# Kernel tuning notes

Measured on AMD Instinct MI355X. Metric: run time of the kernel, lower is better.

Reference implementation:

```python
import jax, jax.numpy as jnp
import numpy as np

M1, M2, BS = 2000, 400, 8
AT = M1 + M2
E1, E2, E3 = 60000, 20000, 20000
H, F, NG, L, C = 64, 64, 50, 4, 4
CUTOFF = 10.0
LOG2 = 0.6931471805599453  # shift of ShiftedSoftplus


def _ssp(x):
    return jax.nn.softplus(x) - LOG2


def _smear(d):
    # GaussianSmearing(0, cutoff, NG)
    offset = jnp.linspace(0.0, CUTOFF, NG)
    coeff = -0.5 / (offset[1] - offset[0]) ** 2
    return jnp.exp(coeff * (d[:, None] - offset[None, :]) ** 2)  # [E, NG]


def _colored_mlp(attr, colors, w1, b1, w2, b2):
    # w1:[C,NG,F] b1:[C,F] w2:[C,F,F] b2:[C,F]; route each edge through its color's MLP
    out = jnp.zeros((attr.shape[0], w1.shape[-1]), attr.dtype)
    for c in range(C):  # fixed small color count
        h = _ssp(attr @ w1[c] + b1[c]) @ w2[c] + b2[c]
        out = out + jnp.where((colors == c)[:, None], h, jnp.zeros((), attr.dtype))
    return out


def _block(h, ei, ew, attr, col, p):
    # InteractionBlock: CFConv -> ssp -> linear
    mw1, mb1, mw2, mb2, cw1, cw2, cb2, bw, bb = p
    Ccut = 0.5 * (jnp.cos(ew * jnp.pi / CUTOFF) + 1.0)
    W = _colored_mlp(attr, col, mw1, mb1, mw2, mb2) * Ccut[:, None]  # [E,F]
    x = h @ cw1                                   # lin1 (no bias) [N,F]
    msg = x[ei[:, 0]] * W                         # gather x_j, modulate
    agg = jax.ops.segment_sum(msg, ei[:, 1], num_segments=h.shape[0])  # scatter-add
    x = agg @ cw2 + cb2                           # lin2
    return _ssp(x) @ bw + bb                      # act + block linear


def _batch_graph(ei, ew, col):
    # replicate per-structure edges across the batch with node offset b*AT
    offs = (jnp.arange(BS, dtype=ei.dtype) * AT)[:, None, None]
    ei_b = (ei[None] + offs).reshape(-1, 2)
    return ei_b, jnp.tile(ew, BS), jnp.tile(col, BS)


def _forward(sites, sites_p, e1, ew1, c1, e2, ew2, c2, e3, ew3, c3,
             emb_w, emb_p_w, mlp_w1, mlp_b1, mlp_w2, mlp_b2,
             conv_w1, conv_w2, conv_b2, blk_w, blk_b,
             out_w1, out_b1, out_w2, out_b2):
    h = jnp.concatenate([emb_w[sites], emb_p_w[sites_p]], axis=1).reshape(BS * AT, H)
    graphs = []
    for (ei, ew, col) in ((e1, ew1, c1), (e2, ew2, c2), (e3, ew3, c3)):
        ei_b, ew_b, col_b = _batch_graph(ei, ew, col)
        graphs.append((ei_b, ew_b, col_b, _smear(ew_b)))
    for l in range(L):
        delta = jnp.zeros_like(h)
        for g, (ei_b, ew_b, col_b, attr_b) in enumerate(graphs):
            p = (mlp_w1[l, g], mlp_b1[l, g], mlp_w2[l, g], mlp_b2[l, g],
                 conv_w1[l, g], conv_w2[l, g], conv_b2[l, g], blk_w[l, g], blk_b[l, g])
            delta = delta + _block(h, ei_b, ew_b, attr_b, col_b, p)
        h = h + delta
    hp = h.reshape(BS, AT, H)[:, M1:, :]   # mask selects pore nodes only
    o = hp @ out_w1 + out_b1               # NB: original has `h - self.act(h)` no-op, so no activation here
    o = o @ out_w2 + out_b2                # [BS, M2, 1]
    return o.sum(axis=1)                   # 'add' readout per batch -> [BS, 1]


def setup_inputs() -> dict:
    key = jax.random.key(0)
    ks = jax.random.split(key, 24)
    f = lambda i, shape, s=0.1: jax.random.normal(ks[i], shape, jnp.float32) * s
    sites = jax.random.randint(ks[0], (BS, M1), 0, 1, dtype=jnp.int32)
    sites_p = jax.random.randint(ks[1], (BS, M2), 0, 2, dtype=jnp.int32)
    e1 = jax.random.randint(ks[2], (E1, 2), 0, M1, dtype=jnp.int32)
    e2 = jnp.stack([jax.random.randint(ks[3], (E2,), 0, M1, dtype=jnp.int32),
                    jax.random.randint(ks[4], (E2,), M1, AT, dtype=jnp.int32)], 1)
    e3 = jnp.stack([jax.random.randint(ks[5], (E3,), M1, AT, dtype=jnp.int32),
                    jax.random.randint(ks[6], (E3,), 0, M1, dtype=jnp.int32)], 1)
    ew1 = jax.random.uniform(ks[7], (E1,), jnp.float32, 0.5, CUTOFF)
    ew2 = jax.random.uniform(ks[8], (E2,), jnp.float32, 0.5, CUTOFF)
    ew3 = jax.random.uniform(ks[9], (E3,), jnp.float32, 0.5, CUTOFF)
    c1 = jax.random.randint(ks[10], (E1,), 0, C, dtype=jnp.int32)
    c2 = jax.random.randint(ks[11], (E2,), 0, C, dtype=jnp.int32)
    c3 = jax.random.randint(ks[12], (E3,), 0, C, dtype=jnp.int32)
    return {
        'sites': sites, 'sites_p': sites_p,
        'edge_idx1': e1, 'edge_weight1': ew1, 'colors1': c1,
        'edge_idx2': e2, 'edge_weight2': ew2, 'colors2': c2,
        'edge_idx3': e3, 'edge_weight3': ew3, 'colors3': c3,
        'emb_w': f(13, (1, H), 1.0), 'emb_p_w': f(14, (2, H), 1.0),
        'mlp_w1': f(15, (L, 3, C, NG, F)), 'mlp_b1': jnp.zeros((L, 3, C, F), jnp.float32),
        'mlp_w2': f(16, (L, 3, C, F, F)), 'mlp_b2': jnp.zeros((L, 3, C, F), jnp.float32),
        'conv_w1': f(17, (L, 3, H, F)), 'conv_w2': f(18, (L, 3, F, H)),
        'conv_b2': jnp.zeros((L, 3, H), jnp.float32),
        'blk_w': f(19, (L, 3, H, H)), 'blk_b': jnp.zeros((L, 3, H), jnp.float32),
        'out_w1': f(20, (H, H // 2)), 'out_b1': jnp.zeros((H // 2,), jnp.float32),
        'out_w2': f(21, (H // 2, 1)), 'out_b2': jnp.zeros((1,), jnp.float32),
    }


def reference(sites, sites_p, edge_idx1, edge_weight1, colors1,
              edge_idx2, edge_weight2, colors2, edge_idx3, edge_weight3, colors3,
              emb_w, emb_p_w, mlp_w1, mlp_b1, mlp_w2, mlp_b2,
              conv_w1, conv_w2, conv_b2, blk_w, blk_b,
              out_w1, out_b1, out_w2, out_b2):
    return _forward(sites, sites_p, edge_idx1, edge_weight1, colors1,
                    edge_idx2, edge_weight2, colors2, edge_idx3, edge_weight3, colors3,
                    emb_w, emb_p_w, mlp_w1, mlp_b1, mlp_w2, mlp_b2,
                    conv_w1, conv_w2, conv_b2, blk_w, blk_b,
                    out_w1, out_b1, out_w2, out_b2)
```

## Files before the change

### kernel.cpp

```cpp
#include <hip/hip_runtime.h>
#include <math.h>

constexpr int M1 = 2000, M2 = 400, BS = 8;
constexpr int AT = M1 + M2;
constexpr int NN = BS * AT;
constexpr int E1 = 60000, E2 = 20000, E3 = 20000;
constexpr int ET = E1 + E2 + E3;
constexpr int H = 64, F = 64, NG = 50, L = 4, C = 4;
constexpr float CUTOFF = 10.0f;
constexpr float LOG2F_ = 0.6931471805599453f;

constexpr float SMEAR_STEP = 10.0f / 49.0f;
constexpr float SMEAR_COEFF = -12.005f;
constexpr float PI_OVER_CUT = 0.31415926535897932f;

constexpr int NBLK = (ET + 255) / 256;

constexpr int NT = 256;
constexpr float DSCALE = (float)(NT - 1) / CUTOFF;

constexpr int GP0 = E1 + 3 * M1;
constexpr int GP1 = E2 + 3 * M2;
constexpr int GP2 = E3 + 3 * M1;
constexpr int ETP = GP0 + GP1 + GP2;

constexpr int TILE_M = 32;

constexpr int GU  = 4400;
constexpr int GBLK = GU / 4;
constexpr int SITE_T = M1 / 4;
constexpr int PORE_T = M2 / 4;
constexpr int NTILE  = SITE_T + PORE_T;

constexpr int LT0 = M1 / 4;
constexpr int LT1 = M1 / 4;
constexpr int LT2 = M2 / 4;
constexpr int LTOT = LT0 + LT1 + LT2;
constexpr int PADB = (3 * AT + 255) / 256;

constexpr int A_TAB  = 192;
constexpr int A_INIT = NN * 64 / 256;
constexpr int A_CNT  = NBLK;
constexpr int A_CV   = 3;
constexpr int A_TOT  = A_TAB + A_INIT + A_CNT + A_CV;
constexpr int B_PACK = 48 * NT * 64 / 256;
constexpr int B_TOT  = B_PACK + 3;

constexpr size_t O_HA    = 0;
constexpr size_t O_HB    = O_HA  + (size_t)NN * 64 * 4;
constexpr size_t O_XG    = O_HB  + (size_t)NN * 64 * 4;
constexpr size_t O_MSG   = O_XG  + (size_t)3 * AT * 512 * 2;
constexpr size_t O_TABF  = O_MSG + (size_t)3 * 8 * AT * 64 * 4;
constexpr size_t O_TAB2  = O_TABF + (size_t)48 * NT * 64 * 4;
constexpr size_t O_EDATA = O_TAB2 + (size_t)48 * NT * 64 * 4;
constexpr size_t O_INT   = O_EDATA + (size_t)ETP * 16;
constexpr int I_DEG  = 0;
constexpr int I_CUR  = 7200;
constexpr int I_ZEND = 14400;
constexpr int I_BASE = 14400;
constexpr int I_CV   = 21616;

__device__ inline float sspf(float x) {
    return fmaxf(x, 0.0f) + log1pf(expf(-fabsf(x))) - LOG2F_;
}
__device__ inline float sspf_fast(float x) {
    float t = __expf(-fabsf(x));
    return fmaxf(x, 0.0f) + __logf(1.0f + t) - LOG2F_;
}

__device__ inline unsigned int bf16rn(float x) {
    unsigned int u = __float_as_uint(x);
    u = (u + 0x7FFFu + ((u >> 16) & 1u)) >> 16;
    return u & 0xFFFFu;
}

__device__ inline int graph_off(int g) { return g == 0 ? 0 : (g == 1 ? GP0 : GP0 + GP1); }

__device__ inline void edge_decode(int idx, int& g, int& e,
                                   const int* ei1, const int* ei2, const int* ei3,
                                   const int* c1, const int* c2, const int* c3,
                                   const int*& ei, const int*& cl) {
    if (idx < E1)            { g = 0; e = idx;           ei = ei1; cl = c1; }
    else if (idx < E1 + E2)  { g = 1; e = idx - E1;      ei = ei2; cl = c2; }
    else                     { g = 2; e = idx - E1 - E2; ei = ei3; cl = c3; }
}

__global__ __launch_bounds__(256) void k_setupA(
    const float* __restrict__ mlp_w1, const float* __restrict__ mlp_b1,
    const float* __restrict__ mlp_w2, const float* __restrict__ mlp_b2,
    float* __restrict__ tabF,
    const int* __restrict__ sites, const int* __restrict__ sites_p,
    const float* __restrict__ emb_w, const float* __restrict__ emb_p_w,
    float* __restrict__ h,
    const int* __restrict__ ei1, const int* __restrict__ ei2,
    const int* __restrict__ ei3, const int* __restrict__ c1,
    const int* __restrict__ c2, const int* __restrict__ c3,
    int* __restrict__ deg,
    const float* __restrict__ conv_b2, const float* __restrict__ blk_w,
    const float* __restrict__ blk_b, float* __restrict__ cvbuf) {
    int bid = blockIdx.x;
    int t = threadIdx.x;
    if (bid < A_TAB) {
        const int lane = t & 63;
        int wslot = bid * 4 + (t >> 6);
        int s = wslot >> 4;
        int pq = wslot & 15;
        int l = s % L;
        int gc = s / L;
        int c = gc % C;
        int g = gc / C;
        size_t wb = (size_t)((l * 3 + g) * C + c);
        const float* w1 = mlp_w1 + wb * NG * F;
        const float* w2 = mlp_w2 + wb * F * F;
        float w1c[NG], w2c[F];
        #pragma unroll
        for (int k = 0; k < NG; k++) w1c[k] = w1[k * F + lane];
        #pragma unroll
        for (int k = 0; k < F; k++) w2c[k] = w2[k * F + lane];
        float b1c = mlp_b1[wb * F + lane];
        float b2c = mlp_b2[wb * F + lane];
        for (int pp = 0; pp < 16; pp++) {
            int p = pq * 16 + pp;
            float d = (float)p * (CUTOFF / (float)(NT - 1));
            float dd = d - (float)lane * SMEAR_STEP;
            float av = (lane < NG) ? __expf(SMEAR_COEFF * dd * dd) : 0.0f;
            float acc = b1c;
            #pragma unroll
            for (int k = 0; k < NG; k++) acc = fmaf(__shfl(av, k), w1c[k], acc);
            float tt = sspf_fast(acc);
            float acc2 = b2c;
            #pragma unroll
            for (int j = 0; j < F; j++) acc2 = fmaf(__shfl(tt, j), w2c[j], acc2);
            float ccut = 0.5f * (__cosf(d * PI_OVER_CUT) + 1.0f);
            tabF[((size_t)s * NT + p) * 64 + lane] = acc2 * ccut;
        }
    } else if (bid < A_TAB + A_INIT) {
        int idx = (bid - A_TAB) * 256 + t;
        int f = idx & 63;
        int n = idx >> 6;
        int b = n / AT;
        int i = n - b * AT;
        float v;
        if (i < M1) v = emb_w[sites[b * M1 + i] * H + f];
        else        v = emb_p_w[sites_p[b * M2 + (i - M1)] * H + f];
        h[idx] = v;
    } else if (bid < A_TAB + A_INIT + A_CNT) {
        int idx = (bid - A_TAB - A_INIT) * 256 + t;
        if (idx < ET) {
            int g, e; const int* ei; const int* cl;
            edge_decode(idx, g, e, ei1, ei2, ei3, c1, c2, c3, ei, cl);
            atomicAdd(&deg[g * AT + ei[2 * e + 1]], 1);
        }
    } else {
        int s = (bid - A_TAB - A_INIT - A_CNT) * 4 + (t >> 6);
        int lane = t & 63;
        if (s < 12) {
            float sl = sspf(conv_b2[s * 64 + lane]);
            const float* bw = blk_w + (size_t)s * 4096;
            float a = blk_b[s * 64 + lane];
            #pragma unroll 8
            for (int k = 0; k < 64; k++)
                a = fmaf(__shfl(sl, k), bw[k * 64 + lane], a);
            cvbuf[s * 64 + lane] = a;
        }
    }
}

__global__ __launch_bounds__(256) void k_setupB(
    const float* __restrict__ tabF, unsigned int* __restrict__ tab2,
    const int* __restrict__ deg, int* __restrict__ base) {
    int bid = blockIdx.x;
    int t = threadIdx.x;
    if (bid < B_PACK) {
        int idx = bid * 256 + t;
        int pc = idx & (NT * 64 - 1);
        int nxt = (pc < (NT - 1) * 64) ? idx + 64 : idx;
        unsigned int lo = bf16rn(tabF[idx]);
        unsigned int hi = bf16rn(tabF[nxt]);
        tab2[idx] = lo | (hi << 16);
    } else {
        const int T = 256, CH = 10;
        __shared__ int lsum[256];
        int g = bid - B_PACK;
        int loc[CH];
        int s = 0;
        #pragma unroll
        for (int i = 0; i < CH; i++) {
            int idx = t * CH + i;
            int v = (idx < AT) ? ((deg[g * AT + idx] + 3) & ~3) : 0;
            loc[i] = s;
            s += v;
        }
        lsum[t] = s;
        __syncthreads();
        for (int off = 1; off < T; off <<= 1) {
            int v = 0;
            if (t >= off) v = lsum[t - off];
            __syncthreads();
            lsum[t] += v;
            __syncthreads();
        }
        int tb = lsum[t] - s;
        #pragma unroll
        for (int i = 0; i < CH; i++) {
            int idx = t * CH + i;
            if (idx < AT) base[g * (AT + 1) + idx] = tb + loc[i];
        }
        if (t == T - 1) base[g * (AT + 1) + AT] = lsum[T - 1];
    }
}

__device__ inline void fma4(float acc[4], float a, const float4 b) {
    acc[0] = fmaf(a, b.x, acc[0]);
    acc[1] = fmaf(a, b.y, acc[1]);
    acc[2] = fmaf(a, b.z, acc[2]);
    acc[3] = fmaf(a, b.w, acc[3]);
}

__device__ inline void stage_B(const float* __restrict__ gB, float (*Bs)[68], int t) {
    #pragma unroll
    for (int i = 0; i < 4; i++) {
        int v = t + i * 256;
        int r = v >> 4, c4 = (v & 15) * 4;
        *(float4*)&Bs[r][c4] = *(const float4*)(gB + (size_t)r * 64 + c4);
    }
}
struct WReg { float4 v0, v1, v2, v3; };
__device__ inline WReg stage_ld(const float* __restrict__ g, int t) {
    int r0 = t >> 4, c4 = (t & 15) * 4;
    WReg w;
    w.v0 = *(const float4*)(g + (size_t)r0 * 64 + c4);
    w.v1 = *(const float4*)(g + (size_t)(r0 + 16) * 64 + c4);
    w.v2 = *(const float4*)(g + (size_t)(r0 + 32) * 64 + c4);
    w.v3 = *(const float4*)(g + (size_t)(r0 + 48) * 64 + c4);
    return w;
}
__device__ inline void stage_st(const WReg& w, float (*Bs)[68], int t) {
    int r0 = t >> 4, c4 = (t & 15) * 4;
    *(float4*)&Bs[r0][c4]      = w.v0;
    *(float4*)&Bs[r0 + 16][c4] = w.v1;
    *(float4*)&Bs[r0 + 32][c4] = w.v2;
    *(float4*)&Bs[r0 + 48][c4] = w.v3;
}

__device__ inline void gemm_tile(const float (*As)[68], const float (*Bs)[68],
                                 int r0, int c0, float acc0[4], float acc1[4]) {
    #pragma unroll 4
    for (int k0 = 0; k0 < 64; k0 += 4) {
        float4 a0 = *(const float4*)&As[r0][k0];
        float4 a1 = *(const float4*)&As[r0 + 1][k0];
        float4 b0 = *(const float4*)&Bs[k0][c0];
        float4 b1 = *(const float4*)&Bs[k0 + 1][c0];
        float4 b2 = *(const float4*)&Bs[k0 + 2][c0];
        float4 b3 = *(const float4*)&Bs[k0 + 3][c0];
        fma4(acc0, a0.x, b0); fma4(acc0, a0.y, b1);
        fma4(acc0, a0.z, b2); fma4(acc0, a0.w, b3);
        fma4(acc1, a1.x, b0); fma4(acc1, a1.y, b1);
        fma4(acc1, a1.z, b2); fma4(acc1, a1.w, b3);
    }
}

__device__ inline void xg_transpose_store(const float (*T)[68],
                                          unsigned short* __restrict__ xg,
                                          int g, int i0, int t) {
    int k = t >> 6, c = t & 63;
    unsigned int w0 = bf16rn(T[k * 8 + 0][c]) | (bf16rn(T[k * 8 + 1][c]) << 16);
    unsigned int w1 = bf16rn(T[k * 8 + 2][c]) | (bf16rn(T[k * 8 + 3][c]) << 16);
    unsigned int w2 = bf16rn(T[k * 8 + 4][c]) | (bf16rn(T[k * 8 + 5][c]) << 16);
    unsigned int w3 = bf16rn(T[k * 8 + 6][c]) | (bf16rn(T[k * 8 + 7][c]) << 16);
    unsigned short* out = xg + (((size_t)g * AT + i0 + k) * 64 + c) * 8;
    *(uint4*)out = make_uint4(w0, w1, w2, w3);
}

__device__ inline float tab_lerp(unsigned int u, int z) {
    float lo = __uint_as_float(u << 16);
    float hi = __uint_as_float(u & 0xFFFF0000u);
    return fmaf(__int_as_float(z), hi - lo, lo);
}
__device__ inline void gmadd8(float acc[8], uint4 q, float wl) {
    acc[0] = fmaf(__uint_as_float(q.x << 16),         wl, acc[0]);
    acc[1] = fmaf(__uint_as_float(q.x & 0xFFFF0000u), wl, acc[1]);
    acc[2] = fmaf(__uint_as_float(q.y << 16),         wl, acc[2]);
    acc[3] = fmaf(__uint_as_float(q.y & 0xFFFF0000u), wl, acc[3]);
    acc[4] = fmaf(__uint_as_float(q.z << 16),         wl, acc[4]);
    acc[5] = fmaf(__uint_as_float(q.z & 0xFFFF0000u), wl, acc[5]);
    acc[6] = fmaf(__uint_as_float(q.w << 16),         wl, acc[6]);
    acc[7] = fmaf(__uint_as_float(q.w & 0xFFFF0000u), wl, acc[7]);
}

__global__ __launch_bounds__(256) void k_gather(
    const int4* __restrict__ edata, const int* __restrict__ base,
    const unsigned int* __restrict__ tab2,
    const unsigned short* __restrict__ xg,
    float* __restrict__ msg, int l) {
    const int t = threadIdx.x;
    const int lane = t & 63;
    const int u = blockIdx.x * 4 + (t >> 6);
    int g, dst;
    if (u < M1)           { g = 0; dst = u; }
    else if (u < AT)      { g = 1; dst = u; }
    else                  { g = 2; dst = u - AT; }
    const int s = base[g * (AT + 1) + dst];
    const int e = base[g * (AT + 1) + dst + 1];
    const int4* ed = edata + graph_off(g);
    const unsigned int* tg = tab2 + ((size_t)g * C * L + l) * NT * 64;
    const unsigned short* xgg = xg + (size_t)g * AT * 512;
    float acc[8];
    #pragma unroll
    for (int j = 0; j < 8; j++) acc[j] = 0.0f;
    for (int i = s; i < e; i += 4) {
        int4 e0 = ed[i];
        int4 e1 = ed[i + 1];
        int4 e2 = ed[i + 2];
        int4 e3 = ed[i + 3];
        unsigned int u0 = tg[(size_t)e0.y * 64 + lane];
        unsigned int u1 = tg[(size_t)e1.y * 64 + lane];
        unsigned int u2 = tg[(size_t)e2.y * 64 + lane];
        unsigned int u3 = tg[(size_t)e3.y * 64 + lane];
        uint4 q0 = *(const uint4*)(xgg + ((size_t)e0.x * 64 + lane) * 8);
        uint4 q1 = *(const uint4*)(xgg + ((size_t)e1.x * 64 + lane) * 8);
        uint4 q2 = *(const uint4*)(xgg + ((size_t)e2.x * 64 + lane) * 8);
        uint4 q3 = *(const uint4*)(xgg + ((size_t)e3.x * 64 + lane) * 8);
        gmadd8(acc, q0, tab_lerp(u0, e0.z));
        gmadd8(acc, q1, tab_lerp(u1, e1.z));
        gmadd8(acc, q2, tab_lerp(u2, e2.z));
        gmadd8(acc, q3, tab_lerp(u3, e3.z));
    }
    float* mp = msg + ((size_t)g * 8 * AT + dst) * 64 + lane;
    #pragma unroll
    for (int b = 0; b < 8; b++) mp[(size_t)b * AT * 64] = acc[b];
}

__global__ __launch_bounds__(256) void k_node(
    const float* __restrict__ msg,
    const float* __restrict__ conv_w2, const float* __restrict__ conv_b2,
    const float* __restrict__ blk_w, const float* __restrict__ blk_b,
    const float* __restrict__ conv_w1, const float* __restrict__ cvbuf,
    const float* __restrict__ hIn, float* __restrict__ hOut,
    unsigned short* __restrict__ xg, int l, int last) {
    __shared__ float As[TILE_M][68];
    __shared__ float Ps[TILE_M][68];
    __shared__ float Bs[64][68];
    const int t = threadIdx.x;
    const int bid = blockIdx.x;
    const int site = (bid < SITE_T) ? 1 : 0;
    const int i0 = site ? bid * 4 : M1 + (bid - SITE_T) * 4;
    const int gA = site ? 0 : 1;
    const size_t pbA = (size_t)(l * 3 + gA);
    const size_t pbB = (size_t)(l * 3 + 2);

    WReg R = stage_ld(conv_w2 + pbA * 4096, t);
    #pragma unroll
    for (int it = 0; it < 2; it++) {
        int v = t + it * 256;
        int r = v >> 4, c4 = (v & 15) * 4;
        int k = r >> 3, b = r & 7;
        *(float4*)&As[r][c4] =
            *(const float4*)(msg + (((size_t)gA * 8 + b) * AT + i0 + k) * 64 + c4);
    }
    stage_st(R, Bs, t);
    R = stage_ld(blk_w + pbA * 4096, t);
    __syncthreads();

    const int cg = t & 15, rg = t >> 4;
    const int c0 = cg * 4, r0 = rg * 2;
    const float* cvl = cvbuf + (size_t)l * 3 * 64;

    float4 cb = *(const float4*)(conv_b2 + pbA * 64 + c0);
    float x0[4] = {cb.x, cb.y, cb.z, cb.w};
    float x1[4] = {cb.x, cb.y, cb.z, cb.w};
    gemm_tile(As, Bs, r0, c0, x0, x1);
    __syncthreads();
    *(float4*)&As[r0][c0] =
        make_float4(sspf(x0[0]), sspf(x0[1]), sspf(x0[2]), sspf(x0[3]));
    *(float4*)&As[r0 + 1][c0] =
        make_float4(sspf(x1[0]), sspf(x1[1]), sspf(x1[2]), sspf(x1[3]));
    stage_st(R, Bs, t);
    if (site) R = stage_ld(conv_w2 + pbB * 4096, t);
    else if (!last) R = stage_ld(conv_w1 + (size_t)((l + 1) * 3 + 2) * 4096, t);
    __syncthreads();

    const int k0r = r0 >> 3, b0r = r0 & 7;
    const size_t o0 = ((size_t)b0r * AT + i0 + k0r) * 64 + c0;
    const int k1r = (r0 + 1) >> 3, b1r = (r0 + 1) & 7;
    const size_t o1 = ((size_t)b1r * AT + i0 + k1r) * 64 + c0;
    float4 h0 = *(const float4*)(hIn + o0);
    float4 h1 = *(const float4*)(hIn + o1);
    float4 bbA = *(const float4*)(blk_b + pbA * 64 + c0);
    float4 ex;
    if (site) {
        float4 bbB = *(const float4*)(blk_b + pbB * 64 + c0);
        float4 cv1 = *(const float4*)(cvl + 64 + c0);
        ex = make_float4(bbB.x + cv1.x, bbB.y + cv1.y, bbB.z + cv1.z, bbB.w + cv1.w);
    } else {
        float4 cv0 = *(const float4*)(cvl + c0);
        float4 cv2 = *(const float4*)(cvl + 128 + c0);
        ex = make_float4(cv0.x + cv2.x, cv0.y + cv2.y, cv0.z + cv2.z, cv0.w + cv2.w);
    }
    float d0[4] = {h0.x + bbA.x + ex.x, h0.y + bbA.y + ex.y,
                   h0.z + bbA.z + ex.z, h0.w + bbA.w + ex.w};
    float d1[4] = {h1.x + bbA.x + ex.x, h1.y + bbA.y + ex.y,
                   h1.z + bbA.z + ex.z, h1.w + bbA.w + ex.w};
    gemm_tile(As, Bs, r0, c0, d0, d1);

    if (site) {
        __syncthreads();
        #pragma unroll
        for (int it = 0; it < 2; it++) {
            int v = t + it * 256;
            int r = v >> 4, c4 = (v & 15) * 4;
            int k = r >> 3, b = r & 7;
            *(float4*)&As[r][c4] =
                *(const float4*)(msg + (((size_t)2 * 8 + b) * AT + i0 + k) * 64 + c4);
        }
        stage_st(R, Bs, t);
        R = stage_ld(blk_w + pbB * 4096, t);
        __syncthreads();
        float4 cb2v = *(const float4*)(conv_b2 + pbB * 64 + c0);
        float y0[4] = {cb2v.x, cb2v.y, cb2v.z, cb2v.w};
        float y1[4] = {cb2v.x, cb2v.y, cb2v.z, cb2v.w};
        gemm_tile(As, Bs, r0, c0, y0, y1);
        __syncthreads();
        *(float4*)&As[r0][c0] =
            make_float4(sspf(y0[0]), sspf(y0[1]), sspf(y0[2]), sspf(y0[3]));
        *(float4*)&As[r0 + 1][c0] =
            make_float4(sspf(y1[0]), sspf(y1[1]), sspf(y1[2]), sspf(y1[3]));
        stage_st(R, Bs, t);
        if (!last) R = stage_ld(conv_w1 + (size_t)((l + 1) * 3 + 0) * 4096, t);
        __syncthreads();
        gemm_tile(As, Bs, r0, c0, d0, d1);
    }
    *(float4*)(hOut + o0) = make_float4(d0[0], d0[1], d0[2], d0[3]);
    *(float4*)(hOut + o1) = make_float4(d1[0], d1[1], d1[2], d1[3]);
    if (last) return;

    __syncthreads();
    *(float4*)&As[r0][c0]     = make_float4(d0[0], d0[1], d0[2], d0[3]);
    *(float4*)&As[r0 + 1][c0] = make_float4(d1[0], d1[1], d1[2], d1[3]);
    stage_st(R, Bs, t);
    if (site) R = stage_ld(conv_w1 + (size_t)((l + 1) * 3 + 1) * 4096, t);
    __syncthreads();
    float p0[4] = {0, 0, 0, 0}, p1[4] = {0, 0, 0, 0};
    gemm_tile(As, Bs, r0, c0, p0, p1);
    __syncthreads();
    *(float4*)&Ps[r0][c0]     = make_float4(p0[0], p0[1], p0[2], p0[3]);
    *(float4*)&Ps[r0 + 1][c0] = make_float4(p1[0], p1[1], p1[2], p1[3]);
    if (site) stage_st(R, Bs, t);
    __syncthreads();
    xg_transpose_store(Ps, xg, site ? 0 : 2, i0, t);
    if (site) {
        float q0[4] = {0, 0, 0, 0}, q1[4] = {0, 0, 0, 0};
        gemm_tile(As, Bs, r0, c0, q0, q1);
        __syncthreads();
        *(float4*)&Ps[r0][c0]     = make_float4(q0[0], q0[1], q0[2], q0[3]);
        *(float4*)&Ps[r0 + 1][c0] = make_float4(q1[0], q1[1], q1[2], q1[3]);
        __syncthreads();
        xg_transpose_store(Ps, xg, 1, i0, t);
    }
}

__global__ __launch_bounds__(256) void k_fl(
    const int* __restrict__ ei1, const int* __restrict__ ei2,
    const int* __restrict__ ei3, const int* __restrict__ c1,
    const int* __restrict__ c2, const int* __restrict__ c3,
    const float* __restrict__ ew1, const float* __restrict__ ew2,
    const float* __restrict__ ew3,
    const int* __restrict__ base, int* __restrict__ cur,
    const int* __restrict__ deg, int4* __restrict__ edata,
    const float* __restrict__ h, const float* __restrict__ conv_w1,
    unsigned short* __restrict__ xg) {
    __shared__ float As[TILE_M][68];
    __shared__ float Bs[64][68];
    int t = threadIdx.x;
    if (blockIdx.x >= LTOT + NBLK) {
        int idx = (blockIdx.x - LTOT - NBLK) * 256 + t;
        if (idx >= 3 * AT) return;
        int g = idx / AT, dn = idx - g * AT;
        int d = deg[g * AT + dn];
        int pd = (d + 3) & ~3;
        int4* ep = edata + graph_off(g) + base[g * (AT + 1) + dn] + d;
        for (int k2 = 0; k2 < pd - d; k2++) ep[k2] = make_int4(0, NT - 1, 0, 0);
        return;
    }
    if (blockIdx.x >= LTOT) {
        int idx = (blockIdx.x - LTOT) * 256 + t;
        if (idx >= ET) return;
        int g, e; const int* ei; const int* cl;
        edge_decode(idx, g, e, ei1, ei2, ei3, c1, c2, c3, ei, cl);
        const float* ew = (g == 0) ? ew1 : (g == 1 ? ew2 : ew3);
        int dst = ei[2 * e + 1];
        int src = ei[2 * e];
        int p = base[g * (AT + 1) + dst] + atomicAdd(&cur[g * AT + dst], 1);
        float tt = ew[e] * DSCALE;
        int i0 = min((int)tt, NT - 2);
        float fr = tt - (float)i0;
        int cb = cl[e] * (L * NT) + i0;
        edata[graph_off(g) + p] = make_int4(src, cb, __float_as_int(fr), 0);
        return;
    }
    int g, igrp;
    {
        int bid = blockIdx.x;
        if (bid < LT0)            { g = 0; igrp = bid; }
        else if (bid < LT0 + LT1) { g = 1; igrp = bid - LT0; }
        else                      { g = 2; igrp = LT0 + (bid - LT0 - LT1); }
    }
    int i0 = igrp * 4;
    #pragma unroll
    for (int it = 0; it < 2; it++) {
        int v = t + it * 256;
        int r = v >> 4, c4 = (v & 15) * 4;
        int n = (r & 7) * AT + i0 + (r >> 3);
        *(float4*)&As[r][c4] = *(const float4*)(h + (size_t)n * 64 + c4);
    }
    stage_B(conv_w1 + (size_t)g * 4096, Bs, t);
    __syncthreads();
    int cg = t & 15, rg = t >> 4;
    int c0 = cg * 4, r0 = rg * 2;
    float acc0[4] = {0, 0, 0, 0}, acc1[4] = {0, 0, 0, 0};
    gemm_tile(As, Bs, r0, c0, acc0, acc1);
    __syncthreads();
    *(float4*)&As[r0][c0]     = make_float4(acc0[0], acc0[1], acc0[2], acc0[3]);
    *(float4*)&As[r0 + 1][c0] = make_float4(acc1[0], acc1[1], acc1[2], acc1[3]);
    __syncthreads();
    xg_transpose_store(As, xg, g, i0, t);
}

__global__ void k_read(const float* __restrict__ h,
                       const float* __restrict__ w1, const float* __restrict__ b1,
                       const float* __restrict__ w2, const float* __restrict__ b2,
                       float* __restrict__ out) {
    int b = blockIdx.x;
    int lane = threadIdx.x & 63;
    int wv = threadIdx.x >> 6;
    __shared__ float part[4];
    float weff = 0.0f;
    #pragma unroll
    for (int j = 0; j < H / 2; j++) weff = fmaf(w1[lane * (H / 2) + j], w2[j], weff);
    float acc = 0.0f;
    for (int i = wv * (M2 / 4); i < (wv + 1) * (M2 / 4); i++)
        acc += h[((size_t)b * AT + M1 + i) * H + lane];
    float v = acc * weff;
    for (int off = 32; off; off >>= 1) v += __shfl_xor(v, off);
    if (lane == 0) part[wv] = v;
    __syncthreads();
    if (threadIdx.x == 0) {
        float bias = b2[0];
        for (int j = 0; j < H / 2; j++) bias = fmaf(b1[j], w2[j], bias);
        out[b] = part[0] + part[1] + part[2] + part[3] + (float)M2 * bias;
    }
}

extern "C" void kernel_launch(void* const* d_in, const int* in_sizes, int n_in,
                              void* d_out, int out_size, void* d_ws, size_t ws_size,
                              hipStream_t stream) {
    const int* sites   = (const int*)d_in[0];
    const int* sites_p = (const int*)d_in[1];
    const int* ei1 = (const int*)d_in[2];
    const float* ew1 = (const float*)d_in[3];
    const int* c1 = (const int*)d_in[4];
    const int* ei2 = (const int*)d_in[5];
    const float* ew2 = (const float*)d_in[6];
    const int* c2 = (const int*)d_in[7];
    const int* ei3 = (const int*)d_in[8];
    const float* ew3 = (const float*)d_in[9];
    const int* c3 = (const int*)d_in[10];
    const float* emb_w   = (const float*)d_in[11];
    const float* emb_p_w = (const float*)d_in[12];
    const float* mlp_w1 = (const float*)d_in[13];
    const float* mlp_b1 = (const float*)d_in[14];
    const float* mlp_w2 = (const float*)d_in[15];
    const float* mlp_b2 = (const float*)d_in[16];
    const float* conv_w1 = (const float*)d_in[17];
    const float* conv_w2 = (const float*)d_in[18];
    const float* conv_b2 = (const float*)d_in[19];
    const float* blk_w = (const float*)d_in[20];
    const float* blk_b = (const float*)d_in[21];
    const float* out_w1 = (const float*)d_in[22];
    const float* out_b1 = (const float*)d_in[23];
    const float* out_w2 = (const float*)d_in[24];
    const float* out_b2 = (const float*)d_in[25];

    char* ws = (char*)d_ws;
    float* hA   = (float*)(ws + O_HA);
    float* hB   = (float*)(ws + O_HB);
    unsigned short* xg = (unsigned short*)(ws + O_XG);
    float* msg  = (float*)(ws + O_MSG);
    float* tabF = (float*)(ws + O_TABF);
    unsigned int* tab2 = (unsigned int*)(ws + O_TAB2);
    int4*  edata = (int4*)(ws + O_EDATA);
    int* ip    = (int*)(ws + O_INT);
    int* deg   = ip + I_DEG;
    int* cur   = ip + I_CUR;
    int* ibase = ip + I_BASE;
    float* cvbuf = (float*)(ip + I_CV);

    hipMemsetAsync(ip, 0, (size_t)I_ZEND * sizeof(int), stream);

    k_setupA<<<A_TOT, 256, 0, stream>>>(mlp_w1, mlp_b1, mlp_w2, mlp_b2, tabF,
                                        sites, sites_p, emb_w, emb_p_w, hA,
                                        ei1, ei2, ei3, c1, c2, c3, deg,
                                        conv_b2, blk_w, blk_b, cvbuf);
    k_setupB<<<B_TOT, 256, 0, stream>>>(tabF, tab2, deg, ibase);
    k_fl<<<LTOT + NBLK + PADB, 256, 0, stream>>>(ei1, ei2, ei3, c1, c2, c3,
                                                 ew1, ew2, ew3, ibase, cur, deg,
                                                 edata, hA, conv_w1, xg);

    float* hcur = hA;
    float* hnxt = hB;
    for (int l = 0; l < L; l++) {
        int last = (l == L - 1) ? 1 : 0;
        k_gather<<<GBLK, 256, 0, stream>>>(edata, ibase, tab2, xg, msg, l);
        k_node<<<NTILE, 256, 0, stream>>>(msg, conv_w2, conv_b2, blk_w, blk_b,
                                          conv_w1, cvbuf, hcur, hnxt, xg, l, last);
        float* tmp = hcur; hcur = hnxt; hnxt = tmp;
    }
    k_read<<<BS, 256, 0, stream>>>(hcur, out_w1, out_b1, out_w2, out_b2, (float*)d_out);
}
```

Before: 327.1 us.

## Fuse setup and per-layer kernels into one persistent cooperative kernel

Merges the setup passes, edge-list build, per-layer gather and node kernels, and the readout into a single cooperative kernel. Stages are separated by grid-wide syncs, and each stage walks its blocks in a grid-stride loop. Only the table-building kernel stays a separate launch. The goal is to remove many kernel launches and the memset. The costs are grid-sync overhead, occupancy capped to a co-resident grid, and higher register/LDS pressure from holding every stage in one kernel.

```diff
diff --git a/kernel.cpp b/kernel.cpp
--- a/kernel.cpp
+++ b/kernel.cpp
@@ -1,5 +1,8 @@
 #include <hip/hip_runtime.h>
+#include <hip/hip_cooperative_groups.h>
 #include <math.h>
+
+namespace cg = cooperative_groups;
 
 constexpr int M1 = 2000, M2 = 400, BS = 8;
 constexpr int AT = M1 + M2;
@@ -40,11 +43,8 @@
 
 constexpr int A_TAB  = 192;
 constexpr int A_INIT = NN * 64 / 256;
-constexpr int A_CNT  = NBLK;
-constexpr int A_CV   = 3;
-constexpr int A_TOT  = A_TAB + A_INIT + A_CNT + A_CV;
 constexpr int B_PACK = 48 * NT * 64 / 256;
-constexpr int B_TOT  = B_PACK + 3;
+constexpr int ZERO_U = (14400 + 255) / 256;
 
 constexpr size_t O_HA    = 0;
 constexpr size_t O_HB    = O_HA  + (size_t)NN * 64 * 4;
@@ -56,7 +56,6 @@
 constexpr size_t O_INT   = O_EDATA + (size_t)ETP * 16;
 constexpr int I_DEG  = 0;
 constexpr int I_CUR  = 7200;
-constexpr int I_ZEND = 14400;
 constexpr int I_BASE = 14400;
 constexpr int I_CV   = 21616;
 
@@ -78,135 +77,50 @@
 
 __device__ inline void edge_decode(int idx, int& g, int& e,
                                    const int* ei1, const int* ei2, const int* ei3,
-                                   const int* c1, const int* c2, const int* c3,
-                                   const int*& ei, const int*& cl) {
+                                   const int*& ei, const int* c1, const int* c2,
+                                   const int* c3, const int*& cl) {
     if (idx < E1)            { g = 0; e = idx;           ei = ei1; cl = c1; }
     else if (idx < E1 + E2)  { g = 1; e = idx - E1;      ei = ei2; cl = c2; }
     else                     { g = 2; e = idx - E1 - E2; ei = ei3; cl = c3; }
 }
 
-__global__ __launch_bounds__(256) void k_setupA(
+__global__ __launch_bounds__(256) void k_tab(
     const float* __restrict__ mlp_w1, const float* __restrict__ mlp_b1,
     const float* __restrict__ mlp_w2, const float* __restrict__ mlp_b2,
-    float* __restrict__ tabF,
-    const int* __restrict__ sites, const int* __restrict__ sites_p,
-    const float* __restrict__ emb_w, const float* __restrict__ emb_p_w,
-    float* __restrict__ h,
-    const int* __restrict__ ei1, const int* __restrict__ ei2,
-    const int* __restrict__ ei3, const int* __restrict__ c1,
-    const int* __restrict__ c2, const int* __restrict__ c3,
-    int* __restrict__ deg,
-    const float* __restrict__ conv_b2, const float* __restrict__ blk_w,
-    const float* __restrict__ blk_b, float* __restrict__ cvbuf) {
-    int bid = blockIdx.x;
-    int t = threadIdx.x;
-    if (bid < A_TAB) {
-        const int lane = t & 63;
-        int wslot = bid * 4 + (t >> 6);
-        int s = wslot >> 4;
-        int pq = wslot & 15;
-        int l = s % L;
-        int gc = s / L;
-        int c = gc % C;
-        int g = gc / C;
-        size_t wb = (size_t)((l * 3 + g) * C + c);
-        const float* w1 = mlp_w1 + wb * NG * F;
-        const float* w2 = mlp_w2 + wb * F * F;
-        float w1c[NG], w2c[F];
+    float* __restrict__ tabF) {
+    const int t = threadIdx.x;
+    const int lane = t & 63;
+    int wslot = blockIdx.x * 4 + (t >> 6);
+    int s = wslot >> 4;
+    int pq = wslot & 15;
+    int l = s % L;
+    int gc = s / L;
+    int c = gc % C;
+    int g = gc / C;
+    size_t wb = (size_t)((l * 3 + g) * C + c);
+    const float* w1 = mlp_w1 + wb * NG * F;
+    const float* w2 = mlp_w2 + wb * F * F;
+    float w1c[NG], w2c[F];
+    #pragma unroll
+    for (int k = 0; k < NG; k++) w1c[k] = w1[k * F + lane];
+    #pragma unroll
+    for (int k = 0; k < F; k++) w2c[k] = w2[k * F + lane];
+    float b1c = mlp_b1[wb * F + lane];
+    float b2c = mlp_b2[wb * F + lane];
+    for (int pp = 0; pp < 16; pp++) {
+        int p = pq * 16 + pp;
+        float d = (float)p * (CUTOFF / (float)(NT - 1));
+        float dd = d - (float)lane * SMEAR_STEP;
+        float av = (lane < NG) ? __expf(SMEAR_COEFF * dd * dd) : 0.0f;
+        float acc = b1c;
         #pragma unroll
-        for (int k = 0; k < NG; k++) w1c[k] = w1[k * F + lane];
+        for (int k = 0; k < NG; k++) acc = fmaf(__shfl(av, k), w1c[k], acc);
+        float tt = sspf_fast(acc);
+        float acc2 = b2c;
         #pragma unroll
-        for (int k = 0; k < F; k++) w2c[k] = w2[k * F + lane];
-        float b1c = mlp_b1[wb * F + lane];
-        float b2c = mlp_b2[wb * F + lane];
-        for (int pp = 0; pp < 16; pp++) {
-            int p = pq * 16 + pp;
-            float d = (float)p * (CUTOFF / (float)(NT - 1));
-            float dd = d - (float)lane * SMEAR_STEP;
-            float av = (lane < NG) ? __expf(SMEAR_COEFF * dd * dd) : 0.0f;
-            float acc = b1c;
-            #pragma unroll
-            for (int k = 0; k < NG; k++) acc = fmaf(__shfl(av, k), w1c[k], acc);
-            float tt = sspf_fast(acc);
-            float acc2 = b2c;
-            #pragma unroll
-            for (int j = 0; j < F; j++) acc2 = fmaf(__shfl(tt, j), w2c[j], acc2);
-            float ccut = 0.5f * (__cosf(d * PI_OVER_CUT) + 1.0f);
-            tabF[((size_t)s * NT + p) * 64 + lane] = acc2 * ccut;
-        }
-    } else if (bid < A_TAB + A_INIT) {
-        int idx = (bid - A_TAB) * 256 + t;
-        int f = idx & 63;
-        int n = idx >> 6;
-        int b = n / AT;
-        int i = n - b * AT;
-        float v;
-        if (i < M1) v = emb_w[sites[b * M1 + i] * H + f];
-        else        v = emb_p_w[sites_p[b * M2 + (i - M1)] * H + f];
-        h[idx] = v;
-    } else if (bid < A_TAB + A_INIT + A_CNT) {
-        int idx = (bid - A_TAB - A_INIT) * 256 + t;
-        if (idx < ET) {
-            int g, e; const int* ei; const int* cl;
-            edge_decode(idx, g, e, ei1, ei2, ei3, c1, c2, c3, ei, cl);
-            atomicAdd(&deg[g * AT + ei[2 * e + 1]], 1);
-        }
-    } else {
-        int s = (bid - A_TAB - A_INIT - A_CNT) * 4 + (t >> 6);
-        int lane = t & 63;
-        if (s < 12) {
-            float sl = sspf(conv_b2[s * 64 + lane]);
-            const float* bw = blk_w + (size_t)s * 4096;
-            float a = blk_b[s * 64 + lane];
-            #pragma unroll 8
-            for (int k = 0; k < 64; k++)
-                a = fmaf(__shfl(sl, k), bw[k * 64 + lane], a);
-            cvbuf[s * 64 + lane] = a;
-        }
-    }
-}
-
-__global__ __launch_bounds__(256) void k_setupB(
-    const float* __restrict__ tabF, unsigned int* __restrict__ tab2,
-    const int* __restrict__ deg, int* __restrict__ base) {
-    int bid = blockIdx.x;
-    int t = threadIdx.x;
-    if (bid < B_PACK) {
-        int idx = bid * 256 + t;
-        int pc = idx & (NT * 64 - 1);
-        int nxt = (pc < (NT - 1) * 64) ? idx + 64 : idx;
-        unsigned int lo = bf16rn(tabF[idx]);
-        unsigned int hi = bf16rn(tabF[nxt]);
-        tab2[idx] = lo | (hi << 16);
-    } else {
-        const int T = 256, CH = 10;
-        __shared__ int lsum[256];
-        int g = bid - B_PACK;
-        int loc[CH];
-        int s = 0;
-        #pragma unroll
-        for (int i = 0; i < CH; i++) {
-            int idx = t * CH + i;
-            int v = (idx < AT) ? ((deg[g * AT + idx] + 3) & ~3) : 0;
-            loc[i] = s;
-            s += v;
-        }
-        lsum[t] = s;
-        __syncthreads();
-        for (int off = 1; off < T; off <<= 1) {
-            int v = 0;
-            if (t >= off) v = lsum[t - off];
-            __syncthreads();
-            lsum[t] += v;
-            __syncthreads();
-        }
-        int tb = lsum[t] - s;
-        #pragma unroll
-        for (int i = 0; i < CH; i++) {
-            int idx = t * CH + i;
-            if (idx < AT) base[g * (AT + 1) + idx] = tb + loc[i];
-        }
-        if (t == T - 1) base[g * (AT + 1) + AT] = lsum[T - 1];
+        for (int j = 0; j < F; j++) acc2 = fmaf(__shfl(tt, j), w2c[j], acc2);
+        float ccut = 0.5f * (__cosf(d * PI_OVER_CUT) + 1.0f);
+        tabF[((size_t)s * NT + p) * 64 + lane] = acc2 * ccut;
     }
 }
 
@@ -216,8 +130,7 @@
     acc[2] = fmaf(a, b.z, acc[2]);
     acc[3] = fmaf(a, b.w, acc[3]);
 }
-
-__device__ inline void stage_B(const float* __restrict__ gB, float (*Bs)[68], int t) {
+__device__ inline void stage_Bs(const float* __restrict__ gB, float (*Bs)[68], int t) {
     #pragma unroll
     for (int i = 0; i < 4; i++) {
         int v = t + i * 256;
@@ -242,7 +155,6 @@
     *(float4*)&Bs[r0 + 32][c4] = w.v2;
     *(float4*)&Bs[r0 + 48][c4] = w.v3;
 }
-
 __device__ inline void gemm_tile(const float (*As)[68], const float (*Bs)[68],
                                  int r0, int c0, float acc0[4], float acc1[4]) {
     #pragma unroll 4
@@ -259,7 +171,6 @@
         fma4(acc1, a1.z, b2); fma4(acc1, a1.w, b3);
     }
 }
-
 __device__ inline void xg_transpose_store(const float (*T)[68],
                                           unsigned short* __restrict__ xg,
                                           int g, int i0, int t) {
@@ -271,7 +182,6 @@
     unsigned short* out = xg + (((size_t)g * AT + i0 + k) * 64 + c) * 8;
     *(uint4*)out = make_uint4(w0, w1, w2, w3);
 }
-
 __device__ inline float tab_lerp(unsigned int u, int z) {
     float lo = __uint_as_float(u << 16);
     float hi = __uint_as_float(u & 0xFFFF0000u);
@@ -288,266 +198,356 @@
     acc[7] = fmaf(__uint_as_float(q.w & 0xFFFF0000u), wl, acc[7]);
 }
 
-__global__ __launch_bounds__(256) void k_gather(
-    const int4* __restrict__ edata, const int* __restrict__ base,
-    const unsigned int* __restrict__ tab2,
-    const unsigned short* __restrict__ xg,
-    float* __restrict__ msg, int l) {
-    const int t = threadIdx.x;
-    const int lane = t & 63;
-    const int u = blockIdx.x * 4 + (t >> 6);
-    int g, dst;
-    if (u < M1)           { g = 0; dst = u; }
-    else if (u < AT)      { g = 1; dst = u; }
-    else                  { g = 2; dst = u - AT; }
-    const int s = base[g * (AT + 1) + dst];
-    const int e = base[g * (AT + 1) + dst + 1];
-    const int4* ed = edata + graph_off(g);
-    const unsigned int* tg = tab2 + ((size_t)g * C * L + l) * NT * 64;
-    const unsigned short* xgg = xg + (size_t)g * AT * 512;
-    float acc[8];
-    #pragma unroll
-    for (int j = 0; j < 8; j++) acc[j] = 0.0f;
-    for (int i = s; i < e; i += 4) {
-        int4 e0 = ed[i];
-        int4 e1 = ed[i + 1];
-        int4 e2 = ed[i + 2];
-        int4 e3 = ed[i + 3];
-        unsigned int u0 = tg[(size_t)e0.y * 64 + lane];
-        unsigned int u1 = tg[(size_t)e1.y * 64 + lane];
-        unsigned int u2 = tg[(size_t)e2.y * 64 + lane];
-        unsigned int u3 = tg[(size_t)e3.y * 64 + lane];
-        uint4 q0 = *(const uint4*)(xgg + ((size_t)e0.x * 64 + lane) * 8);
-        uint4 q1 = *(const uint4*)(xgg + ((size_t)e1.x * 64 + lane) * 8);
-        uint4 q2 = *(const uint4*)(xgg + ((size_t)e2.x * 64 + lane) * 8);
-        uint4 q3 = *(const uint4*)(xgg + ((size_t)e3.x * 64 + lane) * 8);
-        gmadd8(acc, q0, tab_lerp(u0, e0.z));
-        gmadd8(acc, q1, tab_lerp(u1, e1.z));
-        gmadd8(acc, q2, tab_lerp(u2, e2.z));
-        gmadd8(acc, q3, tab_lerp(u3, e3.z));
-    }
-    float* mp = msg + ((size_t)g * 8 * AT + dst) * 64 + lane;
-    #pragma unroll
-    for (int b = 0; b < 8; b++) mp[(size_t)b * AT * 64] = acc[b];
-}
-
-__global__ __launch_bounds__(256) void k_node(
-    const float* __restrict__ msg,
-    const float* __restrict__ conv_w2, const float* __restrict__ conv_b2,
-    const float* __restrict__ blk_w, const float* __restrict__ blk_b,
-    const float* __restrict__ conv_w1, const float* __restrict__ cvbuf,
-    const float* __restrict__ hIn, float* __restrict__ hOut,
-    unsigned short* __restrict__ xg, int l, int last) {
+struct Prm {
+    const int *sites, *sites_p;
+    const int *ei1, *c1, *ei2, *c2, *ei3, *c3;
+    const float *ew1, *ew2, *ew3;
+    const float *emb_w, *emb_p_w;
+    const float *conv_w1, *conv_w2, *conv_b2, *blk_w, *blk_b;
+    const float *out_w1, *out_b1, *out_w2, *out_b2;
+    float *hA, *hB;
+    unsigned short *xg;
+    float *msg;
+    const float *tabF;
+    unsigned int *tab2;
+    int4 *edata;
+    int *ideg, *icur, *ibase;
+    float *cvbuf;
+    float *out;
+};
+
+__global__ __launch_bounds__(256, 4) void k_all(Prm p) {
+    cg::grid_group grid = cg::this_grid();
     __shared__ float As[TILE_M][68];
     __shared__ float Ps[TILE_M][68];
     __shared__ float Bs[64][68];
+    __shared__ int   ls[256];
+    __shared__ float part[4];
     const int t = threadIdx.x;
-    const int bid = blockIdx.x;
-    const int site = (bid < SITE_T) ? 1 : 0;
-    const int i0 = site ? bid * 4 : M1 + (bid - SITE_T) * 4;
-    const int gA = site ? 0 : 1;
-    const size_t pbA = (size_t)(l * 3 + gA);
-    const size_t pbB = (size_t)(l * 3 + 2);
-
-    WReg R = stage_ld(conv_w2 + pbA * 4096, t);
-    #pragma unroll
-    for (int it = 0; it < 2; it++) {
-        int v = t + it * 256;
-        int r = v >> 4, c4 = (v & 15) * 4;
-        int k = r >> 3, b = r & 7;
-        *(float4*)&As[r][c4] =
-            *(const float4*)(msg + (((size_t)gA * 8 + b) * AT + i0 + k) * 64 + c4);
-    }
-    stage_st(R, Bs, t);
-    R = stage_ld(blk_w + pbA * 4096, t);
-    __syncthreads();
-
-    const int cg = t & 15, rg = t >> 4;
-    const int c0 = cg * 4, r0 = rg * 2;
-    const float* cvl = cvbuf + (size_t)l * 3 * 64;
-
-    float4 cb = *(const float4*)(conv_b2 + pbA * 64 + c0);
-    float x0[4] = {cb.x, cb.y, cb.z, cb.w};
-    float x1[4] = {cb.x, cb.y, cb.z, cb.w};
-    gemm_tile(As, Bs, r0, c0, x0, x1);
-    __syncthreads();
-    *(float4*)&As[r0][c0] =
-        make_float4(sspf(x0[0]), sspf(x0[1]), sspf(x0[2]), sspf(x0[3]));
-    *(float4*)&As[r0 + 1][c0] =
-        make_float4(sspf(x1[0]), sspf(x1[1]), sspf(x1[2]), sspf(x1[3]));
-    stage_st(R, Bs, t);
-    if (site) R = stage_ld(conv_w2 + pbB * 4096, t);
-    else if (!last) R = stage_ld(conv_w1 + (size_t)((l + 1) * 3 + 2) * 4096, t);
-    __syncthreads();
-
-    const int k0r = r0 >> 3, b0r = r0 & 7;
-    const size_t o0 = ((size_t)b0r * AT + i0 + k0r) * 64 + c0;
-    const int k1r = (r0 + 1) >> 3, b1r = (r0 + 1) & 7;
-    const size_t o1 = ((size_t)b1r * AT + i0 + k1r) * 64 + c0;
-    float4 h0 = *(const float4*)(hIn + o0);
-    float4 h1 = *(const float4*)(hIn + o1);
-    float4 bbA = *(const float4*)(blk_b + pbA * 64 + c0);
-    float4 ex;
-    if (site) {
-        float4 bbB = *(const float4*)(blk_b + pbB * 64 + c0);
-        float4 cv1 = *(const float4*)(cvl + 64 + c0);
-        ex = make_float4(bbB.x + cv1.x, bbB.y + cv1.y, bbB.z + cv1.z, bbB.w + cv1.w);
-    } else {
-        float4 cv0 = *(const float4*)(cvl + c0);
-        float4 cv2 = *(const float4*)(cvl + 128 + c0);
-        ex = make_float4(cv0.x + cv2.x, cv0.y + cv2.y, cv0.z + cv2.z, cv0.w + cv2.w);
-    }
-    float d0[4] = {h0.x + bbA.x + ex.x, h0.y + bbA.y + ex.y,
-                   h0.z + bbA.z + ex.z, h0.w + bbA.w + ex.w};
-    float d1[4] = {h1.x + bbA.x + ex.x, h1.y + bbA.y + ex.y,
-                   h1.z + bbA.z + ex.z, h1.w + bbA.w + ex.w};
-    gemm_tile(As, Bs, r0, c0, d0, d1);
-
-    if (site) {
-        __syncthreads();
+    const int lane = t & 63;
+    const int wv = t >> 6;
+    const int NB = gridDim.x;
+
+    for (int u = blockIdx.x; u < ZERO_U; u += NB) {
+        int idx = u * 256 + t;
+        if (idx < 14400) p.ideg[idx] = 0;
+    }
+    for (int u = blockIdx.x; u < A_INIT; u += NB) {
+        int idx = u * 256 + t;
+        int f = idx & 63;
+        int n = idx >> 6;
+        int b = n / AT;
+        int i = n - b * AT;
+        float v;
+        if (i < M1) v = p.emb_w[p.sites[b * M1 + i] * H + f];
+        else        v = p.emb_p_w[p.sites_p[b * M2 + (i - M1)] * H + f];
+        p.hA[idx] = v;
+    }
+    for (int u = blockIdx.x; u < 3; u += NB) {
+        int s = u * 4 + wv;
+        float sl = sspf(p.conv_b2[s * 64 + lane]);
+        const float* bw = p.blk_w + (size_t)s * 4096;
+        float a = p.blk_b[s * 64 + lane];
+        #pragma unroll 8
+        for (int k = 0; k < 64; k++)
+            a = fmaf(__shfl(sl, k), bw[k * 64 + lane], a);
+        p.cvbuf[s * 64 + lane] = a;
+    }
+    for (int u = blockIdx.x; u < B_PACK; u += NB) {
+        int idx = u * 256 + t;
+        int pc = idx & (NT * 64 - 1);
+        int nxt = (pc < (NT - 1) * 64) ? idx + 64 : idx;
+        unsigned int lo = bf16rn(p.tabF[idx]);
+        unsigned int hi = bf16rn(p.tabF[nxt]);
+        p.tab2[idx] = lo | (hi << 16);
+    }
+    grid.sync();
+
+    for (int u = blockIdx.x; u < NBLK; u += NB) {
+        int idx = u * 256 + t;
+        if (idx < ET) {
+            int g, e; const int* ei; const int* cl;
+            edge_decode(idx, g, e, p.ei1, p.ei2, p.ei3, ei, p.c1, p.c2, p.c3, cl);
+            atomicAdd(&p.ideg[g * AT + ei[2 * e + 1]], 1);
+        }
+    }
+    for (int u = blockIdx.x; u < LTOT; u += NB) {
+        int g, igrp;
+        if (u < LT0)            { g = 0; igrp = u; }
+        else if (u < LT0 + LT1) { g = 1; igrp = u - LT0; }
+        else                    { g = 2; igrp = LT0 + (u - LT0 - LT1); }
+        int i0 = igrp * 4;
         #pragma unroll
         for (int it = 0; it < 2; it++) {
             int v = t + it * 256;
             int r = v >> 4, c4 = (v & 15) * 4;
-            int k = r >> 3, b = r & 7;
-            *(float4*)&As[r][c4] =
-                *(const float4*)(msg + (((size_t)2 * 8 + b) * AT + i0 + k) * 64 + c4);
-        }
-        stage_st(R, Bs, t);
-        R = stage_ld(blk_w + pbB * 4096, t);
-        __syncthreads();
-        float4 cb2v = *(const float4*)(conv_b2 + pbB * 64 + c0);
-        float y0[4] = {cb2v.x, cb2v.y, cb2v.z, cb2v.w};
-        float y1[4] = {cb2v.x, cb2v.y, cb2v.z, cb2v.w};
-        gemm_tile(As, Bs, r0, c0, y0, y1);
-        __syncthreads();
-        *(float4*)&As[r0][c0] =
-            make_float4(sspf(y0[0]), sspf(y0[1]), sspf(y0[2]), sspf(y0[3]));
-        *(float4*)&As[r0 + 1][c0] =
-            make_float4(sspf(y1[0]), sspf(y1[1]), sspf(y1[2]), sspf(y1[3]));
-        stage_st(R, Bs, t);
-        if (!last) R = stage_ld(conv_w1 + (size_t)((l + 1) * 3 + 0) * 4096, t);
-        __syncthreads();
-        gemm_tile(As, Bs, r0, c0, d0, d1);
-    }
-    *(float4*)(hOut + o0) = make_float4(d0[0], d0[1], d0[2], d0[3]);
-    *(float4*)(hOut + o1) = make_float4(d1[0], d1[1], d1[2], d1[3]);
-    if (last) return;
-
-    __syncthreads();
-    *(float4*)&As[r0][c0]     = make_float4(d0[0], d0[1], d0[2], d0[3]);
-    *(float4*)&As[r0 + 1][c0] = make_float4(d1[0], d1[1], d1[2], d1[3]);
-    stage_st(R, Bs, t);
-    if (site) R = stage_ld(conv_w1 + (size_t)((l + 1) * 3 + 1) * 4096, t);
-    __syncthreads();
-    float p0[4] = {0, 0, 0, 0}, p1[4] = {0, 0, 0, 0};
-    gemm_tile(As, Bs, r0, c0, p0, p1);
-    __syncthreads();
-    *(float4*)&Ps[r0][c0]     = make_float4(p0[0], p0[1], p0[2], p0[3]);
-    *(float4*)&Ps[r0 + 1][c0] = make_float4(p1[0], p1[1], p1[2], p1[3]);
-    if (site) stage_st(R, Bs, t);
-    __syncthreads();
-    xg_transpose_store(Ps, xg, site ? 0 : 2, i0, t);
-    if (site) {
-        float q0[4] = {0, 0, 0, 0}, q1[4] = {0, 0, 0, 0};
-        gemm_tile(As, Bs, r0, c0, q0, q1);
-        __syncthreads();
-        *(float4*)&Ps[r0][c0]     = make_float4(q0[0], q0[1], q0[2], q0[3]);
-        *(float4*)&Ps[r0 + 1][c0] = make_float4(q1[0], q1[1], q1[2], q1[3]);
-        __syncthreads();
-        xg_transpose_store(Ps, xg, 1, i0, t);
-    }
-}
-
-__global__ __launch_bounds__(256) void k_fl(
-    const int* __restrict__ ei1, const int* __restrict__ ei2,
-    const int* __restrict__ ei3, const int* __restrict__ c1,
-    const int* __restrict__ c2, const int* __restrict__ c3,
-    const float* __restrict__ ew1, const float* __restrict__ ew2,
-    const float* __restrict__ ew3,
-    const int* __restrict__ base, int* __restrict__ cur,
-    const int* __restrict__ deg, int4* __restrict__ edata,
-    const float* __restrict__ h, const float* __restrict__ conv_w1,
-    unsigned short* __restrict__ xg) {
-    __shared__ float As[TILE_M][68];
-    __shared__ float Bs[64][68];
-    int t = threadIdx.x;
-    if (blockIdx.x >= LTOT + NBLK) {
-        int idx = (blockIdx.x - LTOT - NBLK) * 256 + t;
-        if (idx >= 3 * AT) return;
-        int g = idx / AT, dn = idx - g * AT;
-        int d = deg[g * AT + dn];
-        int pd = (d + 3) & ~3;
-        int4* ep = edata + graph_off(g) + base[g * (AT + 1) + dn] + d;
-        for (int k2 = 0; k2 < pd - d; k2++) ep[k2] = make_int4(0, NT - 1, 0, 0);
-        return;
-    }
-    if (blockIdx.x >= LTOT) {
-        int idx = (blockIdx.x - LTOT) * 256 + t;
-        if (idx >= ET) return;
-        int g, e; const int* ei; const int* cl;
-        edge_decode(idx, g, e, ei1, ei2, ei3, c1, c2, c3, ei, cl);
-        const float* ew = (g == 0) ? ew1 : (g == 1 ? ew2 : ew3);
-        int dst = ei[2 * e + 1];
-        int src = ei[2 * e];
-        int p = base[g * (AT + 1) + dst] + atomicAdd(&cur[g * AT + dst], 1);
-        float tt = ew[e] * DSCALE;
-        int i0 = min((int)tt, NT - 2);
-        float fr = tt - (float)i0;
-        int cb = cl[e] * (L * NT) + i0;
-        edata[graph_off(g) + p] = make_int4(src, cb, __float_as_int(fr), 0);
-        return;
-    }
-    int g, igrp;
-    {
-        int bid = blockIdx.x;
-        if (bid < LT0)            { g = 0; igrp = bid; }
-        else if (bid < LT0 + LT1) { g = 1; igrp = bid - LT0; }
-        else                      { g = 2; igrp = LT0 + (bid - LT0 - LT1); }
-    }
-    int i0 = igrp * 4;
-    #pragma unroll
-    for (int it = 0; it < 2; it++) {
-        int v = t + it * 256;
-        int r = v >> 4, c4 = (v & 15) * 4;
-        int n = (r & 7) * AT + i0 + (r >> 3);
-        *(float4*)&As[r][c4] = *(const float4*)(h + (size_t)n * 64 + c4);
-    }
-    stage_B(conv_w1 + (size_t)g * 4096, Bs, t);
-    __syncthreads();
-    int cg = t & 15, rg = t >> 4;
-    int c0 = cg * 4, r0 = rg * 2;
-    float acc0[4] = {0, 0, 0, 0}, acc1[4] = {0, 0, 0, 0};
-    gemm_tile(As, Bs, r0, c0, acc0, acc1);
-    __syncthreads();
-    *(float4*)&As[r0][c0]     = make_float4(acc0[0], acc0[1], acc0[2], acc0[3]);
-    *(float4*)&As[r0 + 1][c0] = make_float4(acc1[0], acc1[1], acc1[2], acc1[3]);
-    __syncthreads();
-    xg_transpose_store(As, xg, g, i0, t);
-}
-
-__global__ void k_read(const float* __restrict__ h,
-                       const float* __restrict__ w1, const float* __restrict__ b1,
-                       const float* __restrict__ w2, const float* __restrict__ b2,
-                       float* __restrict__ out) {
-    int b = blockIdx.x;
-    int lane = threadIdx.x & 63;
-    int wv = threadIdx.x >> 6;
-    __shared__ float part[4];
-    float weff = 0.0f;
-    #pragma unroll
-    for (int j = 0; j < H / 2; j++) weff = fmaf(w1[lane * (H / 2) + j], w2[j], weff);
-    float acc = 0.0f;
-    for (int i = wv * (M2 / 4); i < (wv + 1) * (M2 / 4); i++)
-        acc += h[((size_t)b * AT + M1 + i) * H + lane];
-    float v = acc * weff;
-    for (int off = 32; off; off >>= 1) v += __shfl_xor(v, off);
-    if (lane == 0) part[wv] = v;
-    __syncthreads();
-    if (threadIdx.x == 0) {
-        float bias = b2[0];
-        for (int j = 0; j < H / 2; j++) bias = fmaf(b1[j], w2[j], bias);
-        out[b] = part[0] + part[1] + part[2] + part[3] + (float)M2 * bias;
+            int n = (r & 7) * AT + i0 + (r >> 3);
+            *(float4*)&As[r][c4] = *(const float4*)(p.hA + (size_t)n * 64 + c4);
+        }
+        stage_Bs(p.conv_w1 + (size_t)g * 4096, Bs, t);
+        __syncthreads();
+        int cg_ = t & 15, rg = t >> 4;
+        int c0 = cg_ * 4, r0 = rg * 2;
+        float a0[4] = {0, 0, 0, 0}, a1[4] = {0, 0, 0, 0};
+        gemm_tile(As, Bs, r0, c0, a0, a1);
+        __syncthreads();
+        *(float4*)&As[r0][c0]     = make_float4(a0[0], a0[1], a0[2], a0[3]);
+        *(float4*)&As[r0 + 1][c0] = make_float4(a1[0], a1[1], a1[2], a1[3]);
+        __syncthreads();
+        xg_transpose_store(As, p.xg, g, i0, t);
+        __syncthreads();
+    }
+    grid.sync();
+
+    for (int u = blockIdx.x; u < 3; u += NB) {
+        const int CH = 10;
+        int loc[CH];
+        int s = 0;
+        #pragma unroll
+        for (int i = 0; i < CH; i++) {
+            int idx = t * CH + i;
+            int v = (idx < AT) ? ((p.ideg[u * AT + idx] + 3) & ~3) : 0;
+            loc[i] = s;
+            s += v;
+        }
+        ls[t] = s;
+        __syncthreads();
+        for (int off = 1; off < 256; off <<= 1) {
+            int v = 0;
+            if (t >= off) v = ls[t - off];
+            __syncthreads();
+            ls[t] += v;
+            __syncthreads();
+        }
+        int tb = ls[t] - s;
+        #pragma unroll
+        for (int i = 0; i < CH; i++) {
+            int idx = t * CH + i;
+            if (idx < AT) p.ibase[u * (AT + 1) + idx] = tb + loc[i];
+        }
+        if (t == 255) p.ibase[u * (AT + 1) + AT] = ls[255];
+        __syncthreads();
+    }
+    grid.sync();
+
+    for (int u = blockIdx.x; u < NBLK + PADB; u += NB) {
+        if (u < NBLK) {
+            int idx = u * 256 + t;
+            if (idx < ET) {
+                int g, e; const int* ei; const int* cl;
+                edge_decode(idx, g, e, p.ei1, p.ei2, p.ei3, ei, p.c1, p.c2, p.c3, cl);
+                const float* ew = (g == 0) ? p.ew1 : (g == 1 ? p.ew2 : p.ew3);
+                int dst = ei[2 * e + 1];
+                int src = ei[2 * e];
+                int pos = p.ibase[g * (AT + 1) + dst] +
+                          atomicAdd(&p.icur[g * AT + dst], 1);
+                float tt = ew[e] * DSCALE;
+                int i0 = min((int)tt, NT - 2);
+                float fr = tt - (float)i0;
+                int cb = cl[e] * (L * NT) + i0;
+                p.edata[graph_off(g) + pos] = make_int4(src, cb, __float_as_int(fr), 0);
+            }
+        } else {
+            int idx = (u - NBLK) * 256 + t;
+            if (idx < 3 * AT) {
+                int g = idx / AT, dn = idx - g * AT;
+                int d = p.ideg[g * AT + dn];
+                int pd = (d + 3) & ~3;
+                int4* ep = p.edata + graph_off(g) + p.ibase[g * (AT + 1) + dn] + d;
+                for (int k2 = 0; k2 < pd - d; k2++) ep[k2] = make_int4(0, NT - 1, 0, 0);
+            }
+        }
+    }
+    grid.sync();
+
+    float* hbuf0 = p.hA;
+    float* hbuf1 = p.hB;
+    for (int l = 0; l < L; l++) {
+        const int last = (l == L - 1) ? 1 : 0;
+        const float* hIn = hbuf0;
+        float* hOut = hbuf1;
+
+        for (int bu = blockIdx.x; bu < GBLK; bu += NB) {
+            int u = __builtin_amdgcn_readfirstlane(bu * 4 + wv);
+            int g, dst;
+            if (u < M1)      { g = 0; dst = u; }
+            else if (u < AT) { g = 1; dst = u; }
+            else             { g = 2; dst = u - AT; }
+            int s = __builtin_amdgcn_readfirstlane(p.ibase[g * (AT + 1) + dst]);
+            int e = __builtin_amdgcn_readfirstlane(p.ibase[g * (AT + 1) + dst + 1]);
+            const int4* ed = p.edata + graph_off(g);
+            const unsigned int* tg = p.tab2 + ((size_t)g * C * L + l) * NT * 64;
+            const unsigned short* xgg = p.xg + (size_t)g * AT * 512;
+            float acc[8];
+            #pragma unroll
+            for (int j = 0; j < 8; j++) acc[j] = 0.0f;
+            for (int i = s; i < e; i += 4) {
+                int4 e0 = ed[i];
+                int4 e1 = ed[i + 1];
+                int4 e2 = ed[i + 2];
+                int4 e3 = ed[i + 3];
+                unsigned int u0 = tg[(size_t)e0.y * 64 + lane];
+                unsigned int u1 = tg[(size_t)e1.y * 64 + lane];
+                unsigned int u2 = tg[(size_t)e2.y * 64 + lane];
+                unsigned int u3 = tg[(size_t)e3.y * 64 + lane];
+                uint4 q0 = *(const uint4*)(xgg + ((size_t)e0.x * 64 + lane) * 8);
+                uint4 q1 = *(const uint4*)(xgg + ((size_t)e1.x * 64 + lane) * 8);
+                uint4 q2 = *(const uint4*)(xgg + ((size_t)e2.x * 64 + lane) * 8);
+                uint4 q3 = *(const uint4*)(xgg + ((size_t)e3.x * 64 + lane) * 8);
+                gmadd8(acc, q0, tab_lerp(u0, e0.z));
+                gmadd8(acc, q1, tab_lerp(u1, e1.z));
+                gmadd8(acc, q2, tab_lerp(u2, e2.z));
+                gmadd8(acc, q3, tab_lerp(u3, e3.z));
+            }
+            float* mp = p.msg + ((size_t)g * 8 * AT + dst) * 64 + lane;
+            #pragma unroll
+            for (int b = 0; b < 8; b++) mp[(size_t)b * AT * 64] = acc[b];
+        }
+        grid.sync();
+
+        for (int u = blockIdx.x; u < NTILE; u += NB) {
+            const int site = (u < SITE_T) ? 1 : 0;
+            const int i0 = site ? u * 4 : M1 + (u - SITE_T) * 4;
+            const int gA = site ? 0 : 1;
+            const size_t pbA = (size_t)(l * 3 + gA);
+            const size_t pbB = (size_t)(l * 3 + 2);
+
+            WReg R = stage_ld(p.conv_w2 + pbA * 4096, t);
+            #pragma unroll
+            for (int it = 0; it < 2; it++) {
+                int v = t + it * 256;
+                int r = v >> 4, c4 = (v & 15) * 4;
+                int k = r >> 3, b = r & 7;
+                *(float4*)&As[r][c4] = *(const float4*)(
+                    p.msg + (((size_t)gA * 8 + b) * AT + i0 + k) * 64 + c4);
+            }
+            stage_st(R, Bs, t);
+            R = stage_ld(p.blk_w + pbA * 4096, t);
+            __syncthreads();
+
+            const int cg_ = t & 15, rg = t >> 4;
+            const int c0 = cg_ * 4, r0 = rg * 2;
+            const float* cvl = p.cvbuf + (size_t)l * 3 * 64;
+
+            float4 cb = *(const float4*)(p.conv_b2 + pbA * 64 + c0);
+            float x0[4] = {cb.x, cb.y, cb.z, cb.w};
+            float x1[4] = {cb.x, cb.y, cb.z, cb.w};
+            gemm_tile(As, Bs, r0, c0, x0, x1);
+            __syncthreads();
+            *(float4*)&As[r0][c0] =
+                make_float4(sspf(x0[0]), sspf(x0[1]), sspf(x0[2]), sspf(x0[3]));
+            *(float4*)&As[r0 + 1][c0] =
+                make_float4(sspf(x1[0]), sspf(x1[1]), sspf(x1[2]), sspf(x1[3]));
+            stage_st(R, Bs, t);
+            if (site) R = stage_ld(p.conv_w2 + pbB * 4096, t);
+            else if (!last) R = stage_ld(p.conv_w1 + (size_t)((l + 1) * 3 + 2) * 4096, t);
+            __syncthreads();
+
+            const int k0r = r0 >> 3, b0r = r0 & 7;
+            const size_t o0 = ((size_t)b0r * AT + i0 + k0r) * 64 + c0;
+            const int k1r = (r0 + 1) >> 3, b1r = (r0 + 1) & 7;
+            const size_t o1 = ((size_t)b1r * AT + i0 + k1r) * 64 + c0;
+            float4 h0 = *(const float4*)(hIn + o0);
+            float4 h1 = *(const float4*)(hIn + o1);
+            float4 bbA = *(const float4*)(p.blk_b + pbA * 64 + c0);
+            float4 ex;
+            if (site) {
+                float4 bbB = *(const float4*)(p.blk_b + pbB * 64 + c0);
+                float4 cv1 = *(const float4*)(cvl + 64 + c0);
+                ex = make_float4(bbB.x + cv1.x, bbB.y + cv1.y,
+                                 bbB.z + cv1.z, bbB.w + cv1.w);
+            } else {
+                float4 cv0 = *(const float4*)(cvl + c0);
+                float4 cv2 = *(const float4*)(cvl + 128 + c0);
+                ex = make_float4(cv0.x + cv2.x, cv0.y + cv2.y,
+                                 cv0.z + cv2.z, cv0.w + cv2.w);
+            }
+            float d0[4] = {h0.x + bbA.x + ex.x, h0.y + bbA.y + ex.y,
+                           h0.z + bbA.z + ex.z, h0.w + bbA.w + ex.w};
+            float d1[4] = {h1.x + bbA.x + ex.x, h1.y + bbA.y + ex.y,
+                           h1.z + bbA.z + ex.z, h1.w + bbA.w + ex.w};
+            gemm_tile(As, Bs, r0, c0, d0, d1);
+
+            if (site) {
+                __syncthreads();
+                #pragma unroll
+                for (int it = 0; it < 2; it++) {
+                    int v = t + it * 256;
+                    int r = v >> 4, c4 = (v & 15) * 4;
+                    int k = r >> 3, b = r & 7;
+                    *(float4*)&As[r][c4] = *(const float4*)(
+                        p.msg + (((size_t)2 * 8 + b) * AT + i0 + k) * 64 + c4);
+                }
+                stage_st(R, Bs, t);
+                R = stage_ld(p.blk_w + pbB * 4096, t);
+                __syncthreads();
+                float4 cb2v = *(const float4*)(p.conv_b2 + pbB * 64 + c0);
+                float y0[4] = {cb2v.x, cb2v.y, cb2v.z, cb2v.w};
+                float y1[4] = {cb2v.x, cb2v.y, cb2v.z, cb2v.w};
+                gemm_tile(As, Bs, r0, c0, y0, y1);
+                __syncthreads();
+                *(float4*)&As[r0][c0] =
+                    make_float4(sspf(y0[0]), sspf(y0[1]), sspf(y0[2]), sspf(y0[3]));
+                *(float4*)&As[r0 + 1][c0] =
+                    make_float4(sspf(y1[0]), sspf(y1[1]), sspf(y1[2]), sspf(y1[3]));
+                stage_st(R, Bs, t);
+                if (!last) R = stage_ld(p.conv_w1 + (size_t)((l + 1) * 3 + 0) * 4096, t);
+                __syncthreads();
+                gemm_tile(As, Bs, r0, c0, d0, d1);
+            }
+            *(float4*)(hOut + o0) = make_float4(d0[0], d0[1], d0[2], d0[3]);
+            *(float4*)(hOut + o1) = make_float4(d1[0], d1[1], d1[2], d1[3]);
+
+            if (!last) {
+                __syncthreads();
+                *(float4*)&As[r0][c0]     = make_float4(d0[0], d0[1], d0[2], d0[3]);
+                *(float4*)&As[r0 + 1][c0] = make_float4(d1[0], d1[1], d1[2], d1[3]);
+                stage_st(R, Bs, t);
+                if (site) R = stage_ld(p.conv_w1 + (size_t)((l + 1) * 3 + 1) * 4096, t);
+                __syncthreads();
+                float p0[4] = {0, 0, 0, 0}, p1[4] = {0, 0, 0, 0};
+                gemm_tile(As, Bs, r0, c0, p0, p1);
+                __syncthreads();
+                *(float4*)&Ps[r0][c0]     = make_float4(p0[0], p0[1], p0[2], p0[3]);
+                *(float4*)&Ps[r0 + 1][c0] = make_float4(p1[0], p1[1], p1[2], p1[3]);
+                if (site) stage_st(R, Bs, t);
+                __syncthreads();
+                xg_transpose_store(Ps, p.xg, site ? 0 : 2, i0, t);
+                if (site) {
+                    float q0[4] = {0, 0, 0, 0}, q1[4] = {0, 0, 0, 0};
+                    gemm_tile(As, Bs, r0, c0, q0, q1);
+                    __syncthreads();
+                    *(float4*)&Ps[r0][c0]     = make_float4(q0[0], q0[1], q0[2], q0[3]);
+                    *(float4*)&Ps[r0 + 1][c0] = make_float4(q1[0], q1[1], q1[2], q1[3]);
+                    __syncthreads();
+                    xg_transpose_store(Ps, p.xg, 1, i0, t);
+                }
+            }
+            __syncthreads();
+        }
+        grid.sync();
+
+        float* tmp = hbuf0; hbuf0 = hbuf1; hbuf1 = tmp;
+    }
+
+    for (int u = blockIdx.x; u < BS; u += NB) {
+        float weff = 0.0f;
+        #pragma unroll
+        for (int j = 0; j < H / 2; j++)
+            weff = fmaf(p.out_w1[lane * (H / 2) + j], p.out_w2[j], weff);
+        float acc = 0.0f;
+        for (int i = wv * (M2 / 4); i < (wv + 1) * (M2 / 4); i++)
+            acc += hbuf0[((size_t)u * AT + M1 + i) * H + lane];
+        float v = acc * weff;
+        for (int off = 32; off; off >>= 1) v += __shfl_xor(v, off);
+        if (lane == 0) part[wv] = v;
+        __syncthreads();
+        if (t == 0) {
+            float bias = p.out_b2[0];
+            for (int j = 0; j < H / 2; j++) bias = fmaf(p.out_b1[j], p.out_w2[j], bias);
+            p.out[u] = part[0] + part[1] + part[2] + part[3] + (float)M2 * bias;
+        }
+        __syncthreads();
     }
 }
 
@@ -590,30 +590,40 @@
     unsigned int* tab2 = (unsigned int*)(ws + O_TAB2);
     int4*  edata = (int4*)(ws + O_EDATA);
     int* ip    = (int*)(ws + O_INT);
-    int* deg   = ip + I_DEG;
-    int* cur   = ip + I_CUR;
-    int* ibase = ip + I_BASE;
-    float* cvbuf = (float*)(ip + I_CV);
-
-    hipMemsetAsync(ip, 0, (size_t)I_ZEND * sizeof(int), stream);
-
-    k_setupA<<<A_TOT, 256, 0, stream>>>(mlp_w1, mlp_b1, mlp_w2, mlp_b2, tabF,
-                                        sites, sites_p, emb_w, emb_p_w, hA,
-                                        ei1, ei2, ei3, c1, c2, c3, deg,
-                                        conv_b2, blk_w, blk_b, cvbuf);
-    k_setupB<<<B_TOT, 256, 0, stream>>>(tabF, tab2, deg, ibase);
-    k_fl<<<LTOT + NBLK + PADB, 256, 0, stream>>>(ei1, ei2, ei3, c1, c2, c3,
-                                                 ew1, ew2, ew3, ibase, cur, deg,
-                                                 edata, hA, conv_w1, xg);
-
-    float* hcur = hA;
-    float* hnxt = hB;
-    for (int l = 0; l < L; l++) {
-        int last = (l == L - 1) ? 1 : 0;
-        k_gather<<<GBLK, 256, 0, stream>>>(edata, ibase, tab2, xg, msg, l);
-        k_node<<<NTILE, 256, 0, stream>>>(msg, conv_w2, conv_b2, blk_w, blk_b,
-                                          conv_w1, cvbuf, hcur, hnxt, xg, l, last);
-        float* tmp = hcur; hcur = hnxt; hnxt = tmp;
-    }
-    k_read<<<BS, 256, 0, stream>>>(hcur, out_w1, out_b1, out_w2, out_b2, (float*)d_out);
-}
+
+    Prm prm;
+    prm.sites = sites;     prm.sites_p = sites_p;
+    prm.ei1 = ei1; prm.c1 = c1; prm.ei2 = ei2; prm.c2 = c2;
+    prm.ei3 = ei3; prm.c3 = c3;
+    prm.ew1 = ew1; prm.ew2 = ew2; prm.ew3 = ew3;
+    prm.emb_w = emb_w; prm.emb_p_w = emb_p_w;
+    prm.conv_w1 = conv_w1; prm.conv_w2 = conv_w2; prm.conv_b2 = conv_b2;
+    prm.blk_w = blk_w; prm.blk_b = blk_b;
+    prm.out_w1 = out_w1; prm.out_b1 = out_b1;
+    prm.out_w2 = out_w2; prm.out_b2 = out_b2;
+    prm.hA = hA; prm.hB = hB;
+    prm.xg = xg; prm.msg = msg;
+    prm.tabF = tabF; prm.tab2 = tab2;
+    prm.edata = edata;
+    prm.ideg = ip + I_DEG; prm.icur = ip + I_CUR; prm.ibase = ip + I_BASE;
+    prm.cvbuf = (float*)(ip + I_CV);
+    prm.out = (float*)d_out;
+
+    static int coopGrid = 0;
+    if (coopGrid == 0) {
+        int occ = 0;
+        hipOccupancyMaxActiveBlocksPerMultiprocessor(&occ, k_all, 256, 0);
+        hipDeviceProp_t prop;
+        int dev = 0;
+        hipGetDevice(&dev);
+        hipGetDeviceProperties(&prop, dev);
+        long cap = (long)occ * (long)prop.multiProcessorCount;
+        coopGrid = (int)((cap < (long)GBLK) ? cap : (long)GBLK);
+        if (coopGrid < 8) coopGrid = 8;
+    }
+
+    k_tab<<<A_TAB, 256, 0, stream>>>(mlp_w1, mlp_b1, mlp_w2, mlp_b2, tabF);
+    void* args[] = {(void*)&prm};
+    hipLaunchCooperativeKernel((void*)k_all, dim3(coopGrid), dim3(256),
+                               args, 0, stream);
+}
```

After: 1.094 ms. 3.34x slower.
